# Kernel tuning notes

Measured on AMD Instinct MI355X. Metric: run time of the kernel, lower is better.

The kernel has to match this reference:

```python
import jax, jax.numpy as jnp
import numpy as np

N = 8192       # node_num
F_IN = 256     # src_feature
F_OUT = 128    # out_feature
NEG_SLOPE = 0.2  # standard GAT leakyrelu slope
MASK_VAL = -1e12


def setup_inputs() -> dict:
    key = jax.random.key(0)
    k1, k2, k3, k4, k5, k6 = jax.random.split(key, 6)
    x = jax.random.normal(k1, (N, F_IN), dtype=jnp.float32)
    adj = jax.random.randint(k2, (N, N), 0, 2, dtype=jnp.int32)  # 0/1 adjacency mask
    # xavier-uniform-like scales
    W = jax.random.normal(k3, (F_IN, F_OUT), dtype=jnp.float32) * np.float32(1.0 / np.sqrt(F_IN))
    a1 = jax.random.normal(k4, (F_OUT,), dtype=jnp.float32) * np.float32(0.1)  # att[:F_OUT]
    a2 = jax.random.normal(k5, (F_OUT,), dtype=jnp.float32) * np.float32(0.1)  # att[F_OUT:]
    bias = jax.random.normal(k6, (F_OUT,), dtype=jnp.float32) * np.float32(0.1)
    return {"x": x, "adj": adj, "W": W, "a1": a1, "a2": a2, "bias": bias}


def reference(x, adj, W, a1, a2, bias):
    # h = x @ W1  (src_h == dst_h for int src_dst_feature)
    h = x @ W  # [N, F_OUT]
    # e[i,j] = leakyrelu(att^T [h_i || h_j]) decomposed as (h@a1)_i + (h@a2)_j
    s_src = h @ a1  # [N]
    s_dst = h @ a2  # [N]
    e = jax.nn.leaky_relu(s_src[:, None] + s_dst[None, :], NEG_SLOPE)  # [N, N]
    masked = jnp.where(adj > 0, e, jnp.float32(MASK_VAL))
    attention = jax.nn.softmax(masked, axis=1)  # [N, N]
    # dropout in eval mode = identity; aggregate neighbor features
    out = attention @ h + bias  # [N, F_OUT]
    return out
```

## Files before the change

kernel.cpp:

```cpp
#include <hip/hip_runtime.h>
#include <cstdint>
#include <cstddef>

#define NN 8192
#define FIN 256
#define FOUT 128
#define SLOPE 0.2f
#define SHIFT 8.0f

typedef float f32x4 __attribute__((ext_vector_type(4)));
typedef __bf16 bf16x8 __attribute__((ext_vector_type(8)));
typedef int i32x4 __attribute__((ext_vector_type(4)));
typedef unsigned int u32x4 __attribute__((ext_vector_type(4)));

__device__ __forceinline__ unsigned short f2bf(float f) {
  return __builtin_bit_cast(unsigned short, (__bf16)f);
}

__device__ __forceinline__ void async_cp16(void* lds, const void* g) {
  __builtin_amdgcn_global_load_lds(
      (const __attribute__((address_space(1))) void*)g,
      (__attribute__((address_space(3))) void*)lds, 16, 0, 0);
}

__global__ __launch_bounds__(256) void k_pack(const int* __restrict__ adj,
                                              unsigned int* __restrict__ adjp2) {
  const int gw = (blockIdx.x * 256 + threadIdx.x) >> 6;
  const int lane = threadIdx.x & 63;
  #pragma unroll 1
  for (int qt = gw; qt < 8192 * 32; qt += 8192) {
    const int row = qt >> 5;
    const int j256 = qt & 31;
    const int* p = adj + (size_t)row * NN + j256 * 256 + lane;
    const int a0 = p[0];
    const int a1 = p[64];
    const int a2 = p[128];
    const int a3 = p[192];
    const unsigned long long m0 = __ballot(a0 != 0);
    const unsigned long long m1 = __ballot(a1 != 0);
    const unsigned long long m2 = __ballot(a2 != 0);
    const unsigned long long m3 = __ballot(a3 != 0);
    if (lane < 8) {
      const int wg = j256 * 8 + lane;
      const int CB = wg >> 5, ch = (wg >> 1) & 15, w = wg & 1;
      const int RB = row >> 7, r = row & 127;
      const int sel = lane >> 1;
      const unsigned long long mk =
          (sel == 0) ? m0 : (sel == 1) ? m1 : (sel == 2) ? m2 : m3;
      const unsigned int val = (lane & 1) ? (unsigned)(mk >> 32) : (unsigned)mk;
      adjp2[(((size_t)RB * 8 + CB) * 16 + ch) * 256 + w * 128 + r] = val;
    }
  }
}

__global__ __launch_bounds__(256, 4) void k_hw(const float* __restrict__ x,
                                               const float* __restrict__ W,
                                               const float* __restrict__ a1,
                                               const float* __restrict__ a2,
                                               unsigned short* __restrict__ ht,
                                               float* __restrict__ Etab,
                                               unsigned short* __restrict__ FbfF,
                                               unsigned short* __restrict__ FbfF2,
                                               float* __restrict__ outacc,
                                               float* __restrict__ dws) {
  __shared__ float xs[8][256];
  __shared__ unsigned short tile[128][8];
  const int tid = threadIdx.x;
  const int rowbase = blockIdx.x * 8;

  {
    f32x4 z = {0.f, 0.f, 0.f, 0.f};
    *(f32x4*)(outacc + (size_t)blockIdx.x * 1024 + tid * 4) = z;
    if (tid < 2) *(f32x4*)(dws + blockIdx.x * 8 + tid * 4) = z;
  }

  #pragma unroll
  for (int it = 0; it < 2; ++it) {
    int fi = it * 1024 + tid * 4;
    int r = fi >> 8, k = fi & 255;
    *(f32x4*)&xs[r][k] = *(const f32x4*)(x + (size_t)(rowbase + r) * FIN + k);
  }
  __syncthreads();

  const int r = tid >> 5;
  const int cg = tid & 31;
  f32x4 acc = {0.f, 0.f, 0.f, 0.f};

  #pragma unroll 8
  for (int k = 0; k < FIN; ++k) {
    f32x4 wv = *(const f32x4*)(W + k * FOUT + cg * 4);
    float xv = xs[r][k];
    acc[0] += xv * wv[0];
    acc[1] += xv * wv[1];
    acc[2] += xv * wv[2];
    acc[3] += xv * wv[3];
  }

  #pragma unroll
  for (int c = 0; c < 4; ++c) tile[cg * 4 + c][r] = f2bf(acc[c]);

  f32x4 av1 = *(const f32x4*)(a1 + cg * 4);
  f32x4 av2 = *(const f32x4*)(a2 + cg * 4);
  float s1 = acc[0] * av1[0] + acc[1] * av1[1] + acc[2] * av1[2] + acc[3] * av1[3];
  float s2 = acc[0] * av2[0] + acc[1] * av2[1] + acc[2] * av2[2] + acc[3] * av2[3];
  #pragma unroll
  for (int off = 16; off > 0; off >>= 1) {
    s1 += __shfl_xor(s1, off, 64);
    s2 += __shfl_xor(s2, off, 64);
  }
  if (cg == 0) {
    const int row = rowbase + r;
    float c0 = s1 + SHIFT;
    float c = fmaxf(c0, SLOPE * c0);
    Etab[(size_t)row * 2]     = __expf(s1 - c);
    Etab[(size_t)row * 2 + 1] = __expf(SLOPE * s1 - c);
    FbfF[row]  = f2bf(__expf(s2));
    FbfF2[row] = f2bf(__expf(SLOPE * s2));
  }
  __syncthreads();

  if (tid < 128) {
    u32x4 v = *(const u32x4*)&tile[tid][0];
    *(u32x4*)(ht + (size_t)tid * NN + rowbase) = v;
  }
}

__global__ __launch_bounds__(512, 4) void k_gat(const unsigned int* __restrict__ adjp2,
                                                const unsigned short* __restrict__ ht,
                                                const float* __restrict__ Etab,
                                                const unsigned short* __restrict__ FbfF,
                                                const unsigned short* __restrict__ FbfF2,
                                                float* __restrict__ outacc,
                                                float* __restrict__ dws) {
  __shared__ unsigned short sH[2][128 * 64];
  __shared__ unsigned int sAp[2][2][128];
  __shared__ unsigned short sF[2][128];

  const int tid = threadIdx.x;
  const int wave = tid >> 6;
  const int lane = tid & 63;
  const int quad = lane >> 4;
  const int m = lane & 15;
  const int rowbase = (int)(blockIdx.x >> 3) * 128;
  const int colbase = (int)(blockIdx.x & 7) * 1024;
  const int row = rowbase + wave * 16 + m;

  bf16x8 pm, pinv, pones;
  #pragma unroll
  for (int jj = 0; jj < 8; ++jj) {
    pm[jj] = (__bf16)(float)m;
    pinv[jj] = (__bf16)0.03125f;
    pones[jj] = (__bf16)1.0f;
  }
  f32x4 z = {0.f, 0.f, 0.f, 0.f};
  f32x4 rp = __builtin_amdgcn_mfma_f32_16x16x32_bf16(pm, pinv, z, 0, 0, 0);
  f32x4 cp = __builtin_amdgcn_mfma_f32_16x16x32_bf16(pinv, pm, z, 0, 0, 0);
  int rowmap[4], colmap[4];
  #pragma unroll
  for (int r = 0; r < 4; ++r) {
    rowmap[r] = ((int)(rp[r] + 0.5f)) & 15;
    colmap[r] = ((int)(cp[r] + 0.5f)) & 15;
  }

  const float E  = Etab[(size_t)row * 2];
  const float E2 = Etab[(size_t)row * 2 + 1];

  f32x4 acc[8];
  #pragma unroll
  for (int t = 0; t < 8; ++t) acc[t] = z;
  f32x4 den = z;

  const unsigned short* srcH[2];
  #pragma unroll
  for (int il = 0; il < 2; ++il) {
    const int i = wave * 2 + il;
    const int f = i * 8 + (lane >> 3);
    const int g = (lane & 7) ^ (lane >> 3);
    srcH[il] = ht + (size_t)f * NN + colbase + g * 8;
  }
  const unsigned int* srcAp = adjp2 + (size_t)blockIdx.x * 4096 + lane * 4;
  const unsigned short* srcF = nullptr;
  if (wave == 1) {
    srcF = (lane < 8) ? (FbfF + colbase + lane * 8)
                      : (FbfF2 + colbase + (lane - 8) * 8);
  }

  auto stage = [&](int b, int c) {
    #pragma unroll
    for (int il = 0; il < 2; ++il)
      async_cp16(&sH[b][(wave * 2 + il) * 512], srcH[il] + c * 64);
    if (wave == 1 && lane < 16) async_cp16(&sF[b][0], srcF + c * 64);
    if (wave == 2) async_cp16(&sAp[b][0][0], srcAp + c * 256);
  };

  auto compute = [&](int cs) {
    #pragma unroll
    for (int k32 = 0; k32 < 2; ++k32) {
      const unsigned int word = sAp[cs][k32][wave * 16 + m];
      const unsigned int byt = (word >> (quad * 8)) & 0xffu;
      const int jl = k32 * 32 + quad * 8;
      u32x4 Fq = *(const u32x4*)&sF[cs][jl];
      u32x4 Gq = *(const u32x4*)&sF[cs][64 + jl];

      bf16x8 af;
      #pragma unroll
      for (int p = 0; p < 4; ++p) {
        const unsigned fp = Fq[p], gp = Gq[p];
        const float Flo = __builtin_bit_cast(float, fp << 16);
        const float Fhi = __builtin_bit_cast(float, fp & 0xffff0000u);
        const float Glo = __builtin_bit_cast(float, gp << 16);
        const float Ghi = __builtin_bit_cast(float, gp & 0xffff0000u);
        const float wlo = fmaxf(E * Flo, E2 * Glo);
        const float whi = fmaxf(E * Fhi, E2 * Ghi);
        af[p * 2]     = (byt & (1u << (p * 2)))     ? (__bf16)wlo : (__bf16)0.0f;
        af[p * 2 + 1] = (byt & (1u << (p * 2 + 1))) ? (__bf16)whi : (__bf16)0.0f;
      }

      const int s0 = (k32 * 4 + quad) ^ (m & 7);
      #pragma unroll
      for (int t = 0; t < 8; ++t) {
        bf16x8 bt = __builtin_bit_cast(bf16x8,
            *(const u32x4*)&sH[cs][(t * 16 + m) * 64 + s0 * 8]);
        acc[t] = __builtin_amdgcn_mfma_f32_16x16x32_bf16(af, bt, acc[t], 0, 0, 0);
      }
      den = __builtin_amdgcn_mfma_f32_16x16x32_bf16(af, pones, den, 0, 0, 0);
    }
  };

  stage(0, 0);

  #pragma unroll 1
  for (int c = 0; c < 16; c += 2) {
    __syncthreads();
    stage(1, c + 1);
    compute(0);
    __syncthreads();
    if (c + 2 < 16) stage(0, c + 2);
    compute(1);
  }

  #pragma unroll
  for (int r = 0; r < 4; ++r) {
    const int orow = rowbase + wave * 16 + rowmap[r];
    #pragma unroll
    for (int t = 0; t < 8; ++t) {
      atomicAdd(&outacc[(size_t)orow * FOUT + t * 16 + colmap[r]], acc[t][r]);
    }
  }
  if (m == 0) {
    #pragma unroll
    for (int r = 0; r < 4; ++r) {
      atomicAdd(&dws[rowbase + wave * 16 + rowmap[r]], den[r]);
    }
  }
}

__global__ __launch_bounds__(256) void k_fin(const float* __restrict__ dws,
                                             const float* __restrict__ bias,
                                             float* __restrict__ out) {
  const int idx = (blockIdx.x * 256 + threadIdx.x) * 4;
  const int rowi = idx >> 7;
  const int f = idx & 127;
  const float inv = 1.0f / dws[rowi];
  f32x4 v = *(f32x4*)(out + idx);
  f32x4 b = *(const f32x4*)(bias + f);
  v[0] = v[0] * inv + b[0];
  v[1] = v[1] * inv + b[1];
  v[2] = v[2] * inv + b[2];
  v[3] = v[3] * inv + b[3];
  *(f32x4*)(out + idx) = v;
}

extern "C" void kernel_launch(void* const* d_in, const int* in_sizes, int n_in,
                              void* d_out, int out_size, void* d_ws, size_t ws_size,
                              hipStream_t stream) {
  const float* x    = (const float*)d_in[0];
  const int*   adj  = (const int*)d_in[1];
  const float* W    = (const float*)d_in[2];
  const float* a1   = (const float*)d_in[3];
  const float* a2   = (const float*)d_in[4];
  const float* bias = (const float*)d_in[5];
  float* out = (float*)d_out;

  char* ws = (char*)d_ws;
  unsigned short* ht = (unsigned short*)ws;
  float* Etab = (float*)(ws + (size_t)2 * 1024 * 1024);
  unsigned short* FbfF =
      (unsigned short*)(ws + (size_t)2 * 1024 * 1024 + 64 * 1024);
  unsigned short* FbfF2 = FbfF + NN;
  float* dws = (float*)(ws + (size_t)2 * 1024 * 1024 + 96 * 1024);
  unsigned int* adjp2 =
      (unsigned int*)(ws + (size_t)2 * 1024 * 1024 + 128 * 1024);

  k_pack<<<2048, 256, 0, stream>>>(adj, adjp2);
  k_hw<<<NN / 8, 256, 0, stream>>>(x, W, a1, a2, ht, Etab, FbfF, FbfF2, out, dws);
  k_gat<<<512, 512, 0, stream>>>(adjp2, ht, Etab, FbfF, FbfF2, out, dws);
  k_fin<<<(NN * FOUT / 4) / 256, 256, 0, stream>>>(dws, bias, out);
}
```

Measured before the change: 454.4 us.

## Replace atomic output accumulation with per-column-block partials and preload adjacency bits

Each k_gat block now stages its accumulator tile through LDS and writes coalesced partial sums and denominators into a per-column-block workspace. k_fin then reduces the eight partials, which removes the global float atomics and the zero-initialisation in k_hw. The whole adjacency bitmask slice for a block is also loaded once into LDS up front instead of being streamed per chunk. This costs extra workspace traffic, roughly 32 MB of partial writes plus the reads in k_fin, and more LDS per block.

```diff
diff --git a/kernel.cpp b/kernel.cpp
--- a/kernel.cpp
+++ b/kernel.cpp
@@ -60,19 +60,11 @@
                                                unsigned short* __restrict__ ht,
                                                float* __restrict__ Etab,
                                                unsigned short* __restrict__ FbfF,
-                                               unsigned short* __restrict__ FbfF2,
-                                               float* __restrict__ outacc,
-                                               float* __restrict__ dws) {
+                                               unsigned short* __restrict__ FbfF2) {
   __shared__ float xs[8][256];
   __shared__ unsigned short tile[128][8];
   const int tid = threadIdx.x;
   const int rowbase = blockIdx.x * 8;
-
-  {
-    f32x4 z = {0.f, 0.f, 0.f, 0.f};
-    *(f32x4*)(outacc + (size_t)blockIdx.x * 1024 + tid * 4) = z;
-    if (tid < 2) *(f32x4*)(dws + blockIdx.x * 8 + tid * 4) = z;
-  }
 
   #pragma unroll
   for (int it = 0; it < 2; ++it) {
@@ -130,10 +122,10 @@
                                                 const float* __restrict__ Etab,
                                                 const unsigned short* __restrict__ FbfF,
                                                 const unsigned short* __restrict__ FbfF2,
-                                                float* __restrict__ outacc,
-                                                float* __restrict__ dws) {
+                                                float* __restrict__ part,
+                                                float* __restrict__ denp) {
   __shared__ unsigned short sH[2][128 * 64];
-  __shared__ unsigned int sAp[2][2][128];
+  __shared__ unsigned int sAp[16][2][128];
   __shared__ unsigned short sF[2][128];
 
   const int tid = threadIdx.x;
@@ -143,6 +135,7 @@
   const int m = lane & 15;
   const int rowbase = (int)(blockIdx.x >> 3) * 128;
   const int colbase = (int)(blockIdx.x & 7) * 1024;
+  const int CB = (int)(blockIdx.x & 7);
   const int row = rowbase + wave * 16 + m;
 
   bf16x8 pm, pinv, pones;
@@ -178,7 +171,6 @@
     const int g = (lane & 7) ^ (lane >> 3);
     srcH[il] = ht + (size_t)f * NN + colbase + g * 8;
   }
-  const unsigned int* srcAp = adjp2 + (size_t)blockIdx.x * 4096 + lane * 4;
   const unsigned short* srcF = nullptr;
   if (wave == 1) {
     srcF = (lane < 8) ? (FbfF + colbase + lane * 8)
@@ -190,13 +182,12 @@
     for (int il = 0; il < 2; ++il)
       async_cp16(&sH[b][(wave * 2 + il) * 512], srcH[il] + c * 64);
     if (wave == 1 && lane < 16) async_cp16(&sF[b][0], srcF + c * 64);
-    if (wave == 2) async_cp16(&sAp[b][0][0], srcAp + c * 256);
   };
 
-  auto compute = [&](int cs) {
+  auto compute = [&](int cs, int c) {
     #pragma unroll
     for (int k32 = 0; k32 < 2; ++k32) {
-      const unsigned int word = sAp[cs][k32][wave * 16 + m];
+      const unsigned int word = sAp[c][k32][wave * 16 + m];
       const unsigned int byt = (word >> (quad * 8)) & 0xffu;
       const int jl = k32 * 32 + quad * 8;
       u32x4 Fq = *(const u32x4*)&sF[cs][jl];
@@ -227,48 +218,73 @@
     }
   };
 
+  {
+    const unsigned int* srcAp = adjp2 + (size_t)blockIdx.x * 4096;
+    #pragma unroll
+    for (int il = 0; il < 2; ++il)
+      async_cp16(((unsigned int*)sAp) + (wave * 2 + il) * 256,
+                 srcAp + (wave * 2 + il) * 256 + lane * 4);
+  }
   stage(0, 0);
 
   #pragma unroll 1
   for (int c = 0; c < 16; c += 2) {
     __syncthreads();
     stage(1, c + 1);
-    compute(0);
+    compute(0, c);
     __syncthreads();
     if (c + 2 < 16) stage(0, c + 2);
-    compute(1);
-  }
-
-  #pragma unroll
-  for (int r = 0; r < 4; ++r) {
-    const int orow = rowbase + wave * 16 + rowmap[r];
-    #pragma unroll
-    for (int t = 0; t < 8; ++t) {
-      atomicAdd(&outacc[(size_t)orow * FOUT + t * 16 + colmap[r]], acc[t][r]);
+    compute(1, c + 1);
+  }
+
+  float* sOut = (float*)&sH[0][0];
+  #pragma unroll
+  for (int h = 0; h < 2; ++h) {
+    __syncthreads();
+    #pragma unroll
+    for (int r = 0; r < 4; ++r) {
+      #pragma unroll
+      for (int tt = 0; tt < 4; ++tt) {
+        sOut[(wave * 16 + rowmap[r]) * 64 + tt * 16 + colmap[r]] =
+            acc[h * 4 + tt][r];
+      }
     }
+    __syncthreads();
+    #pragma unroll
+    for (int i = 0; i < 4; ++i) {
+      const int v = i * 512 + tid;
+      const int rl = v >> 4, c4 = v & 15;
+      *(f32x4*)&part[((size_t)CB * NN + rowbase + rl) * FOUT + h * 64 + c4 * 4] =
+          ((const f32x4*)sOut)[v];
+    }
   }
   if (m == 0) {
     #pragma unroll
-    for (int r = 0; r < 4; ++r) {
-      atomicAdd(&dws[rowbase + wave * 16 + rowmap[r]], den[r]);
-    }
-  }
-}
-
-__global__ __launch_bounds__(256) void k_fin(const float* __restrict__ dws,
+    for (int r = 0; r < 4; ++r)
+      denp[(size_t)CB * NN + rowbase + wave * 16 + rowmap[r]] = den[r];
+  }
+}
+
+__global__ __launch_bounds__(256) void k_fin(const float* __restrict__ part,
+                                             const float* __restrict__ denp,
                                              const float* __restrict__ bias,
                                              float* __restrict__ out) {
-  const int idx = (blockIdx.x * 256 + threadIdx.x) * 4;
-  const int rowi = idx >> 7;
-  const int f = idx & 127;
-  const float inv = 1.0f / dws[rowi];
-  f32x4 v = *(f32x4*)(out + idx);
+  const int i4 = blockIdx.x * 256 + threadIdx.x;
+  const int rowi = i4 >> 5;
+  const int f = (i4 & 31) * 4;
+  float den = 0.f;
+  f32x4 s = {0.f, 0.f, 0.f, 0.f};
+  #pragma unroll
+  for (int cb = 0; cb < 8; ++cb) {
+    den += denp[(size_t)cb * NN + rowi];
+    f32x4 p = *(const f32x4*)&part[((size_t)cb * NN + rowi) * FOUT + f];
+    s[0] += p[0]; s[1] += p[1]; s[2] += p[2]; s[3] += p[3];
+  }
+  const float inv = 1.0f / den;
   f32x4 b = *(const f32x4*)(bias + f);
-  v[0] = v[0] * inv + b[0];
-  v[1] = v[1] * inv + b[1];
-  v[2] = v[2] * inv + b[2];
-  v[3] = v[3] * inv + b[3];
-  *(f32x4*)(out + idx) = v;
+  f32x4 v = {s[0] * inv + b[0], s[1] * inv + b[1],
+             s[2] * inv + b[2], s[3] * inv + b[3]};
+  *(f32x4*)(out + (size_t)rowi * FOUT + f) = v;
 }
 
 extern "C" void kernel_launch(void* const* d_in, const int* in_sizes, int n_in,
@@ -288,12 +304,13 @@
   unsigned short* FbfF =
       (unsigned short*)(ws + (size_t)2 * 1024 * 1024 + 64 * 1024);
   unsigned short* FbfF2 = FbfF + NN;
-  float* dws = (float*)(ws + (size_t)2 * 1024 * 1024 + 96 * 1024);
   unsigned int* adjp2 =
       (unsigned int*)(ws + (size_t)2 * 1024 * 1024 + 128 * 1024);
+  float* part = (float*)(ws + (size_t)12 * 1024 * 1024);
+  float* denp = (float*)(ws + (size_t)44 * 1024 * 1024);
 
   k_pack<<<2048, 256, 0, stream>>>(adj, adjp2);
-  k_hw<<<NN / 8, 256, 0, stream>>>(x, W, a1, a2, ht, Etab, FbfF, FbfF2, out, dws);
-  k_gat<<<512, 512, 0, stream>>>(adjp2, ht, Etab, FbfF, FbfF2, out, dws);
-  k_fin<<<(NN * FOUT / 4) / 256, 256, 0, stream>>>(dws, bias, out);
-}
+  k_hw<<<NN / 8, 256, 0, stream>>>(x, W, a1, a2, ht, Etab, FbfF, FbfF2);
+  k_gat<<<512, 512, 0, stream>>>(adjp2, ht, Etab, FbfF, FbfF2, part, denp);
+  k_fin<<<(NN * FOUT / 4) / 256, 256, 0, stream>>>(part, denp, bias, out);
+}
```

Result: faster. 442.1 us (-2.7%).
